# Optimization experiments

Hardware: AMD Instinct MI355X
Metric: run time of the kernel (lower is better)

## Reference

```python
import jax, jax.numpy as jnp
import numpy as np

B, SQ, SK, DQ, DKV, DH, DV = 8, 2048, 2048, 1024, 1024, 1024, 1024


def setup_inputs() -> dict:
    ks = jax.random.split(jax.random.key(0), 10)
    q = jax.random.normal(ks[0], (B, SQ, DQ), dtype=jnp.float32)
    k = jax.random.normal(ks[1], (B, SK, DKV), dtype=jnp.float32)
    v = jax.random.normal(ks[2], (B, SK, DKV), dtype=jnp.float32)
    mask = jax.random.randint(ks[3], (B, SK), 0, 2).astype(jnp.bool_)
    s = 1.0 / np.sqrt(DQ)
    Wq = jax.random.normal(ks[4], (DQ, DH), dtype=jnp.float32) * s
    bq = jnp.zeros((DH,), dtype=jnp.float32)
    Wk = jax.random.normal(ks[5], (DKV, DH), dtype=jnp.float32) * s
    bk = jnp.zeros((DH,), dtype=jnp.float32)
    Wv = jax.random.normal(ks[6], (DKV, DV), dtype=jnp.float32) * s
    bv = jnp.zeros((DV,), dtype=jnp.float32)
    return {"q": q, "k": k, "v": v, "mask": mask,
            "Wq": Wq, "bq": bq, "Wk": Wk, "bk": bk, "Wv": Wv, "bv": bv}


def reference(q, k, v, mask, Wq, bq, Wk, bk, Wv, bv):
    # Linear projections
    Qp = q @ Wq + bq                       # [B, SQ, DH]
    Kp = k @ Wk + bk                       # [B, SK, DH]
    Vp = jnp.tanh(v @ Wv + bv)             # [B, SK, DV] (value has Tanh)
    # Scores; NOTE: original adds the *bool* mask, i.e. +0/+1, not -inf masking
    qk = jnp.einsum('bqd,bkd->bqk', Qp, Kp)
    qk = qk + mask[:, None, :].astype(qk.dtype)   # broadcast of mask.unsqueeze(1)
    attn = jax.nn.softmax(qk, axis=-1)
    out = jnp.einsum('bqk,bkd->bqd', attn, Vp)    # [B, SQ, DV]
    return out
```

## Files before the change

### kernel.cpp

```cpp
#include <hip/hip_runtime.h>
#include <math.h>

#define BB 8
#define SQL 2048
#define SKL 2048
#define DD 1024

typedef __attribute__((ext_vector_type(8))) short bf16x8;
typedef __attribute__((ext_vector_type(4))) float f32x4;
typedef __attribute__((ext_vector_type(4))) unsigned short us4;
typedef unsigned short u16;

__device__ __forceinline__ u16 f2bf(float f) {
    unsigned u = __float_as_uint(f);
    u += 0x7fffu + ((u >> 16) & 1u);
    return (u16)(u >> 16);
}
__device__ __forceinline__ float bf2f(u16 h) {
    return __uint_as_float((unsigned)h << 16);
}

__global__ __launch_bounds__(256)
void split3(const float* __restrict__ in, u16* __restrict__ oh,
            u16* __restrict__ ol, long n4) {
    long i = (long)blockIdx.x * 256 + threadIdx.x;
    if (i >= n4) return;
    float4 v = ((const float4*)in)[i];
    us4 h, l;
    h.x = f2bf(v.x); l.x = f2bf(v.x - bf2f(h.x));
    h.y = f2bf(v.y); l.y = f2bf(v.y - bf2f(h.y));
    h.z = f2bf(v.z); l.z = f2bf(v.z - bf2f(h.z));
    h.w = f2bf(v.w); l.w = f2bf(v.w - bf2f(h.w));
    ((us4*)oh)[i] = h;
    ((us4*)ol)[i] = l;
}

__global__ __launch_bounds__(256)
void splitT3(const float* __restrict__ W, u16* __restrict__ WhT,
             u16* __restrict__ WlT) {
    __shared__ float t[32][33];
    const int n0 = blockIdx.x * 32, k0 = blockIdx.y * 32;
    const int tx = threadIdx.x & 31, ty = threadIdx.x >> 5;
#pragma unroll
    for (int r = 0; r < 32; r += 8)
        t[ty + r][tx] = W[(long)(k0 + ty + r) * DD + n0 + tx];
    __syncthreads();
#pragma unroll
    for (int r = 0; r < 32; r += 8) {
        float x = t[tx][ty + r];
        u16 h = f2bf(x);
        WhT[(long)(n0 + ty + r) * DD + k0 + tx] = h;
        WlT[(long)(n0 + ty + r) * DD + k0 + tx] = f2bf(x - bf2f(h));
    }
}

#define GLL(gp, lp) __builtin_amdgcn_global_load_lds( \
    (const __attribute__((address_space(1))) void*)(gp), \
    (__attribute__((address_space(3))) void*)(lp), 16, 0, 0)

__global__ __launch_bounds__(256, 2)
void gemm3(const u16* __restrict__ Ah, const u16* __restrict__ Al,
           const u16* __restrict__ Bh, const u16* __restrict__ Bl,
           int lda, int ldb, int K, long sA, long sB,
           const float* __restrict__ bias, const int* __restrict__ mask, int sM,
           float* __restrict__ Cf, u16* __restrict__ C1, u16* __restrict__ C2,
           long sC, int ldc, int mode)
{
    __shared__ u16 AsH[4096], AsL[4096], BsH[4096], BsL[4096];

    const int z = blockIdx.z;
    const long zA = (long)z * sA, zB = (long)z * sB;
    const int tid = threadIdx.x, lane = tid & 63, wave = tid >> 6;
    const int wm = (wave & 1) * 64, wn = (wave >> 1) * 64;
    const int l15 = lane & 15, lq = lane >> 4;
    const long row0 = (long)blockIdx.y * 128, col0 = (long)blockIdx.x * 128;

    long offA[2], offB[2]; int lds[2];
#pragma unroll
    for (int it = 0; it < 2; it++) {
        int c = tid + it * 256, row = c >> 2;
        int qg = (c & 3) ^ ((row >> 1) & 3);
        offA[it] = (row0 + row) * (long)lda + qg * 8;
        offB[it] = (col0 + row) * (long)ldb + qg * 8;
        lds[it] = c * 8;
    }

    int aoff[4], boff[4];
#pragma unroll
    for (int i = 0; i < 4; i++) {
        int r = wm + i * 16 + l15;
        aoff[i] = r * 32 + ((lq ^ ((r >> 1) & 3)) * 8);
    }
#pragma unroll
    for (int j = 0; j < 4; j++) {
        int r = wn + j * 16 + l15;
        boff[j] = r * 32 + ((lq ^ ((r >> 1) & 3)) * 8);
    }

    f32x4 acc[4][4];
#pragma unroll
    for (int i = 0; i < 4; i++)
#pragma unroll
        for (int j = 0; j < 4; j++)
#pragma unroll
            for (int e = 0; e < 4; e++) acc[i][j][e] = 0.f;

    for (int k0 = 0; k0 < K; k0 += 32) {
#pragma unroll
        for (int it = 0; it < 2; it++) {
            GLL(Ah + zA + offA[it] + k0, AsH + lds[it]);
            GLL(Al + zA + offA[it] + k0, AsL + lds[it]);
            GLL(Bh + zB + offB[it] + k0, BsH + lds[it]);
            GLL(Bl + zB + offB[it] + k0, BsL + lds[it]);
        }
        __syncthreads();

        bf16x8 ah[4], al[4], bh[4], bl[4];
#pragma unroll
        for (int i = 0; i < 4; i++) {
            ah[i] = *(const bf16x8*)(AsH + aoff[i]);
            al[i] = *(const bf16x8*)(AsL + aoff[i]);
        }
#pragma unroll
        for (int j = 0; j < 4; j++) {
            bh[j] = *(const bf16x8*)(BsH + boff[j]);
            bl[j] = *(const bf16x8*)(BsL + boff[j]);
        }
#pragma unroll
        for (int i = 0; i < 4; i++)
#pragma unroll
            for (int j = 0; j < 4; j++) {
                acc[i][j] = __builtin_amdgcn_mfma_f32_16x16x32_bf16(ah[i], bh[j], acc[i][j], 0, 0, 0);
                acc[i][j] = __builtin_amdgcn_mfma_f32_16x16x32_bf16(ah[i], bl[j], acc[i][j], 0, 0, 0);
                acc[i][j] = __builtin_amdgcn_mfma_f32_16x16x32_bf16(al[i], bh[j], acc[i][j], 0, 0, 0);
            }
        __syncthreads();
    }

    const long zc = (long)z * sC;
#pragma unroll
    for (int i = 0; i < 4; i++) {
#pragma unroll
        for (int j = 0; j < 4; j++) {
            const long col = col0 + wn + j * 16 + l15;
            const long rbase = row0 + wm + i * 16 + lq * 4;
            if (mode == 0 || mode == 3) {
                const float madd = (mode == 3) ? (float)mask[(long)z * sM + col] : 0.f;
#pragma unroll
                for (int r = 0; r < 4; r++)
                    Cf[zc + (rbase + r) * (long)ldc + col] = acc[i][j][r] + madd;
            } else if (mode == 1) {
                const float bv = bias[col];
#pragma unroll
                for (int r = 0; r < 4; r++) {
                    float val = acc[i][j][r] + bv;
                    u16 h = f2bf(val);
                    C1[zc + (rbase + r) * (long)ldc + col] = h;
                    C2[zc + (rbase + r) * (long)ldc + col] = f2bf(val - bf2f(h));
                }
            } else {
                const float bv = bias[col];
                us4 o;
                o.x = f2bf(tanhf(acc[i][j][0] + bv));
                o.y = f2bf(tanhf(acc[i][j][1] + bv));
                o.z = f2bf(tanhf(acc[i][j][2] + bv));
                o.w = f2bf(tanhf(acc[i][j][3] + bv));
                *(us4*)(C1 + zc + col * (long)ldc + rbase) = o;
            }
        }
    }
}

__global__ __launch_bounds__(256, 2)
void gemm1(const u16* __restrict__ A, const u16* __restrict__ B,
           float* __restrict__ C, int lda, int ldb, int K,
           long sA, long sB, long sC, int ldc)
{
    __shared__ u16 As[4096], Bs[4096];

    const int z = blockIdx.z;
    const long zA = (long)z * sA, zB = (long)z * sB;
    const int tid = threadIdx.x, lane = tid & 63, wave = tid >> 6;
    const int wm = (wave & 1) * 64, wn = (wave >> 1) * 64;
    const int l15 = lane & 15, lq = lane >> 4;
    const long row0 = (long)blockIdx.y * 128, col0 = (long)blockIdx.x * 128;

    long offA[2], offB[2]; int lds[2];
#pragma unroll
    for (int it = 0; it < 2; it++) {
        int c = tid + it * 256, row = c >> 2;
        int qg = (c & 3) ^ ((row >> 1) & 3);
        offA[it] = (row0 + row) * (long)lda + qg * 8;
        offB[it] = (col0 + row) * (long)ldb + qg * 8;
        lds[it] = c * 8;
    }
    int aoff[4], boff[4];
#pragma unroll
    for (int i = 0; i < 4; i++) {
        int r = wm + i * 16 + l15;
        aoff[i] = r * 32 + ((lq ^ ((r >> 1) & 3)) * 8);
    }
#pragma unroll
    for (int j = 0; j < 4; j++) {
        int r = wn + j * 16 + l15;
        boff[j] = r * 32 + ((lq ^ ((r >> 1) & 3)) * 8);
    }

    f32x4 acc[4][4];
#pragma unroll
    for (int i = 0; i < 4; i++)
#pragma unroll
        for (int j = 0; j < 4; j++)
#pragma unroll
            for (int e = 0; e < 4; e++) acc[i][j][e] = 0.f;

    for (int k0 = 0; k0 < K; k0 += 32) {
#pragma unroll
        for (int it = 0; it < 2; it++) {
            GLL(A + zA + offA[it] + k0, As + lds[it]);
            GLL(B + zB + offB[it] + k0, Bs + lds[it]);
        }
        __syncthreads();
        bf16x8 af[4], bf[4];
#pragma unroll
        for (int i = 0; i < 4; i++) af[i] = *(const bf16x8*)(As + aoff[i]);
#pragma unroll
        for (int j = 0; j < 4; j++) bf[j] = *(const bf16x8*)(Bs + boff[j]);
#pragma unroll
        for (int i = 0; i < 4; i++)
#pragma unroll
            for (int j = 0; j < 4; j++)
                acc[i][j] = __builtin_amdgcn_mfma_f32_16x16x32_bf16(af[i], bf[j], acc[i][j], 0, 0, 0);
        __syncthreads();
    }

    const long zc = (long)z * sC;
#pragma unroll
    for (int i = 0; i < 4; i++)
#pragma unroll
        for (int j = 0; j < 4; j++) {
            const long col = col0 + wn + j * 16 + l15;
            const long rbase = row0 + wm + i * 16 + lq * 4;
#pragma unroll
            for (int r = 0; r < 4; r++)
                C[zc + (rbase + r) * (long)ldc + col] = acc[i][j][r];
        }
}

__global__ __launch_bounds__(256)
void softmax_bf(float* __restrict__ S)
{
    float* p = S + (long)blockIdx.x * SKL;
    u16* po = (u16*)S + (long)blockIdx.x * 2 * SKL;
    const int tid = threadIdx.x;
    const int w = tid >> 6, lane = tid & 63;

    float4 v0 = *(float4*)(p + tid * 8);
    float4 v1 = *(float4*)(p + tid * 8 + 4);

    float m = fmaxf(fmaxf(fmaxf(v0.x, v0.y), fmaxf(v0.z, v0.w)),
                    fmaxf(fmaxf(v1.x, v1.y), fmaxf(v1.z, v1.w)));
#pragma unroll
    for (int off = 32; off; off >>= 1) m = fmaxf(m, __shfl_down(m, off));

    __shared__ float wm_[4], ws_[4];
    if (lane == 0) wm_[w] = m;
    __syncthreads();
    const float bm = fmaxf(fmaxf(wm_[0], wm_[1]), fmaxf(wm_[2], wm_[3]));

    v0.x = __expf(v0.x - bm); v0.y = __expf(v0.y - bm);
    v0.z = __expf(v0.z - bm); v0.w = __expf(v0.w - bm);
    v1.x = __expf(v1.x - bm); v1.y = __expf(v1.y - bm);
    v1.z = __expf(v1.z - bm); v1.w = __expf(v1.w - bm);

    float s = v0.x + v0.y + v0.z + v0.w + v1.x + v1.y + v1.z + v1.w;
#pragma unroll
    for (int off = 32; off; off >>= 1) s += __shfl_down(s, off);
    if (lane == 0) ws_[w] = s;
    __syncthreads();
    const float inv = 1.f / (ws_[0] + ws_[1] + ws_[2] + ws_[3]);

    us4 o0, o1;
    o0.x = f2bf(v0.x * inv); o0.y = f2bf(v0.y * inv);
    o0.z = f2bf(v0.z * inv); o0.w = f2bf(v0.w * inv);
    o1.x = f2bf(v1.x * inv); o1.y = f2bf(v1.y * inv);
    o1.z = f2bf(v1.z * inv); o1.w = f2bf(v1.w * inv);
    *(us4*)(po + tid * 8) = o0;
    *(us4*)(po + tid * 8 + 4) = o1;
}

extern "C" void kernel_launch(void* const* d_in, const int* in_sizes, int n_in,
                              void* d_out, int out_size, void* d_ws, size_t ws_size,
                              hipStream_t stream)
{
    const float* q  = (const float*)d_in[0];
    const float* k  = (const float*)d_in[1];
    const float* v  = (const float*)d_in[2];
    const int* mask = (const int*)d_in[3];
    const float* Wq = (const float*)d_in[4];
    const float* bq = (const float*)d_in[5];
    const float* Wk = (const float*)d_in[6];
    const float* bk = (const float*)d_in[7];
    const float* Wv = (const float*)d_in[8];
    const float* bv = (const float*)d_in[9];
    float* out = (float*)d_out;

    const long PZ = (long)SKL * DD;
    u16*   KpH = (u16*)d_ws;
    u16*   KpL = KpH + BB * PZ;
    u16*   Vt  = KpL + BB * PZ;
    float* S   = (float*)(Vt + BB * PZ);
    u16*   inH = (u16*)S;
    u16*   inL = inH + BB * PZ;
    u16*   WhT = inL + BB * PZ;
    u16*   WlT = WhT + (long)DD * DD;
    u16*   QpH = (u16*)d_out;
    u16*   QpL = QpH + BB * PZ;
    u16*   P   = (u16*)S;

    const dim3 b256(256);
    const long n4 = BB * PZ / 4;
    const dim3 gSplit((unsigned)(n4 / 256));
    const dim3 gW(32, 32);
    const dim3 gProj(8, 16, BB);
    const dim3 gQK(16, 16, BB);
    const dim3 gPV(8, 16, BB);
    const dim3 gSm(BB * SQL);

    split3<<<gSplit, b256, 0, stream>>>(q, inH, inL, n4);
    splitT3<<<gW, b256, 0, stream>>>(Wq, WhT, WlT);
    gemm3<<<gProj, b256, 0, stream>>>(inH, inL, WhT, WlT, DD, DD, DD, PZ, 0,
                                      bq, nullptr, 0, nullptr, QpH, QpL, PZ, DD, 1);
    split3<<<gSplit, b256, 0, stream>>>(k, inH, inL, n4);
    splitT3<<<gW, b256, 0, stream>>>(Wk, WhT, WlT);
    gemm3<<<gProj, b256, 0, stream>>>(inH, inL, WhT, WlT, DD, DD, DD, PZ, 0,
                                      bk, nullptr, 0, nullptr, KpH, KpL, PZ, DD, 1);
    split3<<<gSplit, b256, 0, stream>>>(v, inH, inL, n4);
    splitT3<<<gW, b256, 0, stream>>>(Wv, WhT, WlT);
    gemm3<<<gProj, b256, 0, stream>>>(inH, inL, WhT, WlT, DD, DD, DD, PZ, 0,
                                      bv, nullptr, 0, nullptr, Vt, nullptr, PZ, SKL, 2);
    gemm3<<<gQK, b256, 0, stream>>>(QpH, QpL, KpH, KpL, DD, DD, DD, PZ, PZ,
                                    nullptr, mask, SKL,
                                    S, nullptr, nullptr, (long)SQL * SKL, SKL, 3);
    softmax_bf<<<gSm, b256, 0, stream>>>(S);
    gemm1<<<gPV, b256, 0, stream>>>(P, Vt, out, 2 * SKL, SKL, SKL,
                                    (long)SQL * 2 * SKL, PZ,
                                    (long)SQL * DD, DD);
}
```

Before: 975.7 us.

## Enlarge gemm3 to 256x256 tiles with double-buffered LDS prefetch pipeline

The split-bf16 gemm3 kernel moves from 128x128 tiles with 256 threads to 256x256 tiles with 512 threads and a 128KB LDS double buffer. The next k-slice is loaded directly into LDS while MFMAs run on the current one, with split waitcnt barriers and raised wave priority around the MFMA phases. This is meant to hide global load latency and raise operand reuse per tile. In exchange it needs more LDS and registers (acc is now 8x4 per wave), which likely limits the kernel to one block per CU and produces fewer blocks for the projection GEMMs.

New measurement: 850.5 us. 12.8% less time.

```diff
diff --git a/kernel.cpp b/kernel.cpp
--- a/kernel.cpp
+++ b/kernel.cpp
@@ -58,7 +58,7 @@
     (const __attribute__((address_space(1))) void*)(gp), \
     (__attribute__((address_space(3))) void*)(lp), 16, 0, 0)
 
-__global__ __launch_bounds__(256, 2)
+__global__ __launch_bounds__(512, 2)
 void gemm3(const u16* __restrict__ Ah, const u16* __restrict__ Al,
            const u16* __restrict__ Bh, const u16* __restrict__ Bl,
            int lda, int ldb, int K, long sA, long sB,
@@ -66,84 +66,113 @@
            float* __restrict__ Cf, u16* __restrict__ C1, u16* __restrict__ C2,
            long sC, int ldc, int mode)
 {
-    __shared__ u16 AsH[4096], AsL[4096], BsH[4096], BsL[4096];
+    __shared__ u16 L[65536];
 
     const int z = blockIdx.z;
     const long zA = (long)z * sA, zB = (long)z * sB;
     const int tid = threadIdx.x, lane = tid & 63, wave = tid >> 6;
-    const int wm = (wave & 1) * 64, wn = (wave >> 1) * 64;
+    const int wm = wave >> 2, wn = wave & 3;
     const int l15 = lane & 15, lq = lane >> 4;
-    const long row0 = (long)blockIdx.y * 128, col0 = (long)blockIdx.x * 128;
-
-    long offA[2], offB[2]; int lds[2];
-#pragma unroll
-    for (int it = 0; it < 2; it++) {
-        int c = tid + it * 256, row = c >> 2;
-        int qg = (c & 3) ^ ((row >> 1) & 3);
-        offA[it] = (row0 + row) * (long)lda + qg * 8;
-        offB[it] = (col0 + row) * (long)ldb + qg * 8;
-        lds[it] = c * 8;
-    }
-
-    int aoff[4], boff[4];
-#pragma unroll
-    for (int i = 0; i < 4; i++) {
-        int r = wm + i * 16 + l15;
-        aoff[i] = r * 32 + ((lq ^ ((r >> 1) & 3)) * 8);
+    const long row0 = (long)blockIdx.y * 256, col0 = (long)blockIdx.x * 256;
+
+    const int pl = tid >> 8;
+    const int c = tid & 255;
+    const int srow = c >> 2;
+    const int qg = (c & 3) ^ ((srow >> 1) & 3);
+    const u16* sAp = (pl ? Al : Ah) + zA + qg * 8;
+    const u16* sBp = (pl ? Bl : Bh) + zB + qg * 8;
+    int ofA[4], ofB[4];
+#pragma unroll
+    for (int p = 0; p < 4; p++) {
+        ofA[p] = (int)((row0 + p * 64 + srow) * (long)lda);
+        ofB[p] = (int)((col0 + p * 64 + srow) * (long)ldb);
+    }
+    const int dst = tid * 8;
+
+#define STB(p, kk, bb) GLL(sBp + ofB[p] + (kk), L + (bb) + 16384 + (p) * 4096 + dst)
+#define STA(p, kk, bb) GLL(sAp + ofA[p] + (kk), L + (bb) + (p) * 4096 + dst)
+
+    int aoff[8], boff[4];
+#pragma unroll
+    for (int i = 0; i < 8; i++) {
+        int r = wm * 128 + i * 16 + l15;
+        aoff[i] = (r >> 6) * 4096 + (r & 63) * 32 + ((lq ^ ((r >> 1) & 3)) * 8);
     }
 #pragma unroll
     for (int j = 0; j < 4; j++) {
-        int r = wn + j * 16 + l15;
-        boff[j] = r * 32 + ((lq ^ ((r >> 1) & 3)) * 8);
-    }
-
-    f32x4 acc[4][4];
-#pragma unroll
-    for (int i = 0; i < 4; i++)
+        int r = wn * 64 + j * 16 + l15;
+        boff[j] = 16384 + (r >> 6) * 4096 + (r & 63) * 32 + ((lq ^ ((r >> 1) & 3)) * 8);
+    }
+
+    f32x4 acc[8][4];
+#pragma unroll
+    for (int i = 0; i < 8; i++)
 #pragma unroll
         for (int j = 0; j < 4; j++)
 #pragma unroll
             for (int e = 0; e < 4; e++) acc[i][j][e] = 0.f;
 
-    for (int k0 = 0; k0 < K; k0 += 32) {
-#pragma unroll
-        for (int it = 0; it < 2; it++) {
-            GLL(Ah + zA + offA[it] + k0, AsH + lds[it]);
-            GLL(Al + zA + offA[it] + k0, AsL + lds[it]);
-            GLL(Bh + zB + offB[it] + k0, BsH + lds[it]);
-            GLL(Bl + zB + offB[it] + k0, BsL + lds[it]);
-        }
-        __syncthreads();
-
-        bf16x8 ah[4], al[4], bh[4], bl[4];
-#pragma unroll
-        for (int i = 0; i < 4; i++) {
-            ah[i] = *(const bf16x8*)(AsH + aoff[i]);
-            al[i] = *(const bf16x8*)(AsL + aoff[i]);
-        }
+#define PHASE(mh) do { \
+    bf16x8 xh[4], xl[4], yh[4], yl[4]; \
+    _Pragma("unroll") \
+    for (int ii = 0; ii < 4; ii++) { \
+        xh[ii] = *(const bf16x8*)(L + bo + aoff[(mh) * 4 + ii]); \
+        xl[ii] = *(const bf16x8*)(L + bo + aoff[(mh) * 4 + ii] + 2048); \
+    } \
+    _Pragma("unroll") \
+    for (int j = 0; j < 4; j++) { \
+        yh[j] = *(const bf16x8*)(L + bo + boff[j]); \
+        yl[j] = *(const bf16x8*)(L + bo + boff[j] + 2048); \
+    } \
+    __builtin_amdgcn_s_setprio(1); \
+    _Pragma("unroll") \
+    for (int ii = 0; ii < 4; ii++) { \
+        _Pragma("unroll") \
+        for (int j = 0; j < 4; j++) { \
+            f32x4 t_ = acc[(mh) * 4 + ii][j]; \
+            t_ = __builtin_amdgcn_mfma_f32_16x16x32_bf16(xh[ii], yh[j], t_, 0, 0, 0); \
+            t_ = __builtin_amdgcn_mfma_f32_16x16x32_bf16(xh[ii], yl[j], t_, 0, 0, 0); \
+            t_ = __builtin_amdgcn_mfma_f32_16x16x32_bf16(xl[ii], yh[j], t_, 0, 0, 0); \
+            acc[(mh) * 4 + ii][j] = t_; \
+        } \
+    } \
+    __builtin_amdgcn_s_setprio(0); \
+} while (0)
+
+    const int NT = K >> 5;
+    STB(0, 0, 0); STB(1, 0, 0); STB(2, 0, 0); STB(3, 0, 0);
+    STA(0, 0, 0); STA(2, 0, 0); STA(1, 0, 0); STA(3, 0, 0);
+
+    for (int t = 0; t < NT; ++t) {
+        const int bo = (t & 1) << 15;
+        const int bn = bo ^ 32768;
+        const int kn = (t + 1) << 5;
+        const bool pf = (t + 1) < NT;
+
+        asm volatile("s_waitcnt vmcnt(2)" ::: "memory");
+        __builtin_amdgcn_s_barrier();
+        __builtin_amdgcn_sched_barrier(0);
+        if (pf) { STB(0, kn, bn); STB(1, kn, bn); STB(2, kn, bn); STB(3, kn, bn); }
+        PHASE(0);
+
+        if (pf) asm volatile("s_waitcnt vmcnt(4)" ::: "memory");
+        else    asm volatile("s_waitcnt vmcnt(0)" ::: "memory");
+        __builtin_amdgcn_s_barrier();
+        __builtin_amdgcn_sched_barrier(0);
+        if (pf) { STA(0, kn, bn); STA(2, kn, bn); STA(1, kn, bn); STA(3, kn, bn); }
+        PHASE(1);
+    }
+#undef PHASE
+#undef STA
+#undef STB
+
+    const long zc = (long)z * sC;
+#pragma unroll
+    for (int i = 0; i < 8; i++) {
 #pragma unroll
         for (int j = 0; j < 4; j++) {
-            bh[j] = *(const bf16x8*)(BsH + boff[j]);
-            bl[j] = *(const bf16x8*)(BsL + boff[j]);
-        }
-#pragma unroll
-        for (int i = 0; i < 4; i++)
-#pragma unroll
-            for (int j = 0; j < 4; j++) {
-                acc[i][j] = __builtin_amdgcn_mfma_f32_16x16x32_bf16(ah[i], bh[j], acc[i][j], 0, 0, 0);
-                acc[i][j] = __builtin_amdgcn_mfma_f32_16x16x32_bf16(ah[i], bl[j], acc[i][j], 0, 0, 0);
-                acc[i][j] = __builtin_amdgcn_mfma_f32_16x16x32_bf16(al[i], bh[j], acc[i][j], 0, 0, 0);
-            }
-        __syncthreads();
-    }
-
-    const long zc = (long)z * sC;
-#pragma unroll
-    for (int i = 0; i < 4; i++) {
-#pragma unroll
-        for (int j = 0; j < 4; j++) {
-            const long col = col0 + wn + j * 16 + l15;
-            const long rbase = row0 + wm + i * 16 + lq * 4;
+            const long col = col0 + wn * 64 + j * 16 + l15;
+            const long rbase = row0 + wm * 128 + i * 16 + lq * 4;
             if (mode == 0 || mode == 3) {
                 const float madd = (mode == 3) ? (float)mask[(long)z * sM + col] : 0.f;
 #pragma unroll
@@ -318,28 +347,28 @@
     u16*   QpL = QpH + BB * PZ;
     u16*   P   = (u16*)S;
 
-    const dim3 b256(256);
+    const dim3 b256(256), b512(512);
     const long n4 = BB * PZ / 4;
     const dim3 gSplit((unsigned)(n4 / 256));
     const dim3 gW(32, 32);
-    const dim3 gProj(8, 16, BB);
-    const dim3 gQK(16, 16, BB);
+    const dim3 gProj(DD / 256, SQL / 256, BB);
+    const dim3 gQK(SKL / 256, SQL / 256, BB);
     const dim3 gPV(8, 16, BB);
     const dim3 gSm(BB * SQL);
 
     split3<<<gSplit, b256, 0, stream>>>(q, inH, inL, n4);
     splitT3<<<gW, b256, 0, stream>>>(Wq, WhT, WlT);
-    gemm3<<<gProj, b256, 0, stream>>>(inH, inL, WhT, WlT, DD, DD, DD, PZ, 0,
+    gemm3<<<gProj, b512, 0, stream>>>(inH, inL, WhT, WlT, DD, DD, DD, PZ, 0,
                                       bq, nullptr, 0, nullptr, QpH, QpL, PZ, DD, 1);
     split3<<<gSplit, b256, 0, stream>>>(k, inH, inL, n4);
     splitT3<<<gW, b256, 0, stream>>>(Wk, WhT, WlT);
-    gemm3<<<gProj, b256, 0, stream>>>(inH, inL, WhT, WlT, DD, DD, DD, PZ, 0,
+    gemm3<<<gProj, b512, 0, stream>>>(inH, inL, WhT, WlT, DD, DD, DD, PZ, 0,
                                       bk, nullptr, 0, nullptr, KpH, KpL, PZ, DD, 1);
     split3<<<gSplit, b256, 0, stream>>>(v, inH, inL, n4);
     splitT3<<<gW, b256, 0, stream>>>(Wv, WhT, WlT);
-    gemm3<<<gProj, b256, 0, stream>>>(inH, inL, WhT, WlT, DD, DD, DD, PZ, 0,
+    gemm3<<<gProj, b512, 0, stream>>>(inH, inL, WhT, WlT, DD, DD, DD, PZ, 0,
                                       bv, nullptr, 0, nullptr, Vt, nullptr, PZ, SKL, 2);
-    gemm3<<<gQK, b256, 0, stream>>>(QpH, QpL, KpH, KpL, DD, DD, DD, PZ, PZ,
+    gemm3<<<gQK, b512, 0, stream>>>(QpH, QpL, KpH, KpL, DD, DD, DD, PZ, PZ,
                                     nullptr, mask, SKL,
                                     S, nullptr, nullptr, (long)SQL * SKL, SKL, 3);
     softmax_bf<<<gSm, b256, 0, stream>>>(S);
```
